# Optimization experiments

Hardware: AMD Instinct MI355X
Metric: run time of the kernel (lower is better)

The kernel has to match this reference:

```python
import jax, jax.numpy as jnp
import numpy as np

HEADS = 8
DIM_HEAD = 64
NB_FEATURES = 256
DIM = 512

def setup_inputs() -> dict:
    key = jax.random.key(0)
    ks = jax.random.split(key, 4)
    b, n = 2, 8192
    x = jax.random.normal(ks[0], (b, n, DIM), jnp.float32)
    # fan-in scaling so exp(feature projections) stays numerically sane
    Wqkv = jax.random.normal(ks[1], (3 * HEADS * DIM_HEAD, DIM), jnp.float32) / np.sqrt(DIM).astype(np.float32)
    Wout = jax.random.normal(ks[2], (DIM, HEADS * DIM_HEAD), jnp.float32) / np.sqrt(HEADS * DIM_HEAD).astype(np.float32)
    bout = jnp.zeros((DIM,), jnp.float32)
    proj = jax.random.normal(ks[3], (NB_FEATURES, DIM_HEAD), jnp.float32) / np.sqrt(DIM_HEAD).astype(np.float32)
    return {"x": x, "Wqkv": Wqkv, "Wout": Wout, "bout": bout, "proj": proj}

def reference(x, Wqkv, Wout, bout, proj):
    b, n, _ = x.shape
    scale = DIM_HEAD ** -0.5
    qkv = jnp.einsum('bnd,ed->bne', x, Wqkv)            # [b,n,3*h*dh]
    q, k, v = jnp.split(qkv, 3, axis=-1)
    to_heads = lambda t: t.reshape(b, n, HEADS, DIM_HEAD).transpose(0, 2, 1, 3)  # [b,h,n,dh]
    q = to_heads(q) * scale
    k = to_heads(k)
    v = to_heads(v)
    # FAVOR+ exp feature maps
    q_prime = jnp.exp(jnp.einsum('bhnd,fd->bhnf', q, proj))  # [b,h,n,f]
    k_prime = jnp.exp(jnp.einsum('bhnd,fd->bhnf', k, proj))  # [b,h,n,f]
    k_sum = k_prime.sum(axis=2)                              # [b,h,f]
    D = jnp.einsum('bhnf,bhf->bhn', q_prime, k_sum)          # normalizer
    D_inv = 1.0 / (D + 1e-6)
    context = jnp.einsum('bhmf,bhmd->bhfd', k_prime, v)      # [b,h,f,dh]
    out = jnp.einsum('bhnf,bhfd->bhnd', q_prime, context) * D_inv[..., None]
    out = out.transpose(0, 2, 1, 3).reshape(b, n, HEADS * DIM_HEAD)
    return jnp.einsum('bne,de->bnd', out, Wout) + bout
```

## Files before the change

### kernel.cpp

```cpp
#include <hip/hip_runtime.h>
#include <math.h>

#define B_    2
#define NSEQ  8192
#define DIM_  512
#define H_    8
#define DH_   64
#define F_    256
#define M_    (B_*NSEQ)
#define QKV_  1536

typedef __attribute__((ext_vector_type(8))) short     short8;
typedef __attribute__((ext_vector_type(4))) float     float4v;
typedef __attribute__((ext_vector_type(8))) unsigned short ushort8v;

__device__ __forceinline__ unsigned short f2bf(float f) {
    unsigned u = __float_as_uint(f);
    u += 0x7FFFu + ((u >> 16) & 1u);
    return (unsigned short)(u >> 16);
}
__device__ __forceinline__ unsigned pack2bf(float lo, float hi) {
    return __builtin_amdgcn_perm(__float_as_uint(hi), __float_as_uint(lo), 0x07060302);
}
__device__ __forceinline__ void glds16(const void* g, void* s) {
    __builtin_amdgcn_global_load_lds(
        (const __attribute__((address_space(1))) unsigned int*)g,
        (__attribute__((address_space(3))) unsigned int*)s, 16, 0, 0);
}

__global__ __launch_bounds__(256) void cvt_all(const float* __restrict__ x,
                                               const float* __restrict__ wqkv,
                                               const float* __restrict__ wout,
                                               const float* __restrict__ proj,
                                               unsigned short* __restrict__ xb,
                                               unsigned short* __restrict__ wqkvb,
                                               unsigned short* __restrict__ woutb,
                                               unsigned short* __restrict__ projb) {
    int bid = blockIdx.x;
    const float* in; unsigned short* out; int i;
    if (bid < 4096)      { in = x;    out = xb;    i = bid * 256 + threadIdx.x; }
    else if (bid < 4480) { in = wqkv; out = wqkvb; i = (bid - 4096) * 256 + threadIdx.x; }
    else if (bid < 4608) { in = wout; out = woutb; i = (bid - 4480) * 256 + threadIdx.x; }
    else                 { in = proj; out = projb; i = (bid - 4608) * 256 + threadIdx.x; }
    float4 a = ((const float4*)in)[2 * i];
    float4 b = ((const float4*)in)[2 * i + 1];
    ushort8v o;
    o[0] = f2bf(a.x); o[1] = f2bf(a.y); o[2] = f2bf(a.z); o[3] = f2bf(a.w);
    o[4] = f2bf(b.x); o[5] = f2bf(b.y); o[6] = f2bf(b.z); o[7] = f2bf(b.w);
    ((ushort8v*)out)[i] = o;
}

template<bool BF16OUT>
__global__ __launch_bounds__(256) void gemm_nt_pp(const unsigned short* __restrict__ A,
                                                  const unsigned short* __restrict__ Bm,
                                                  const float* __restrict__ bias,
                                                  void* __restrict__ Cout,
                                                  int M, int N, int K) {
    __shared__ __align__(16) unsigned short As[2][128 * 32];
    __shared__ __align__(16) unsigned short Bs[2][128 * 32];
    const int t  = threadIdx.x;
    const int w  = t >> 6, l = t & 63;
    const int wm = w >> 1, wn = w & 1;
    const int m0 = blockIdx.y * 128, n0 = blockIdx.x * 128;
    const int lr = l & 15, lq = l >> 4;

    float4v acc[4][4];
#pragma unroll
    for (int mi = 0; mi < 4; mi++)
#pragma unroll
        for (int ni = 0; ni < 4; ni++) acc[mi][ni] = (float4v){0.f, 0.f, 0.f, 0.f};

    auto stage = [&](int buf, int k0) {
#pragma unroll
        for (int i = 0; i < 2; i++) {
            int rb8 = w * 2 + i;
            int row = rb8 * 16 + lr;
            glds16(A + (size_t)(m0 + row) * K + k0 + lq * 8, &As[buf][rb8 * 512]);
            glds16(Bm + (size_t)(n0 + row) * K + k0 + lq * 8, &Bs[buf][rb8 * 512]);
        }
    };

    const int nk = K >> 5;
    stage(0, 0);
    __syncthreads();

    for (int k = 0; k < nk; k++) {
        const int cur = k & 1;
        if (k + 1 < nk) stage(cur ^ 1, (k + 1) << 5);

        short8 af[4], bfr[4];
#pragma unroll
        for (int mi = 0; mi < 4; mi++)
            af[mi] = *(const short8*)&As[cur][((wm * 4 + mi) * 64 + l) * 8];
#pragma unroll
        for (int ni = 0; ni < 4; ni++)
            bfr[ni] = *(const short8*)&Bs[cur][((wn * 4 + ni) * 64 + l) * 8];
#pragma unroll
        for (int mi = 0; mi < 4; mi++)
#pragma unroll
            for (int ni = 0; ni < 4; ni++)
                acc[mi][ni] = __builtin_amdgcn_mfma_f32_16x16x32_bf16(
                    af[mi], bfr[ni], acc[mi][ni], 0, 0, 0);

        if (k + 1 < nk) __syncthreads();
    }

    const int q = l >> 4, c = l & 15;
#pragma unroll
    for (int mi = 0; mi < 4; mi++) {
        int row0 = m0 + wm * 64 + mi * 16 + q * 4;
#pragma unroll
        for (int ni = 0; ni < 4; ni++) {
            int col = n0 + wn * 64 + ni * 16 + c;
            float bv = bias ? bias[col] : 0.f;
#pragma unroll
            for (int r = 0; r < 4; r++) {
                float v = acc[mi][ni][r] + bv;
                if (BF16OUT) ((unsigned short*)Cout)[(size_t)(row0 + r) * N + col] = f2bf(v);
                else         ((float*)Cout)[(size_t)(row0 + r) * N + col] = v;
            }
        }
    }
}

__global__ __launch_bounds__(256) void vtrans(const unsigned short* __restrict__ qkvb,
                                              unsigned short* __restrict__ vT) {
    __shared__ unsigned short T[128][80];
    const int t = threadIdx.x;
    const int n0 = blockIdx.x * 128, z = blockIdx.y;
    const int b = z >> 3, h = z & 7;
#pragma unroll
    for (int i = 0; i < 4; i++) {
        int flat = t + i * 256;
        int n = flat >> 3, d8 = flat & 7;
        ushort8v v = *(const ushort8v*)(qkvb + ((size_t)b * NSEQ + n0 + n) * QKV_ + 1024 + h * 64 + d8 * 8);
        *(ushort8v*)&T[n][d8 * 8] = v;
    }
    __syncthreads();
#pragma unroll
    for (int i = 0; i < 4; i++) {
        int flat = t + i * 256;
        int d = flat >> 4, n8 = flat & 15;
        ushort8v o;
#pragma unroll
        for (int j = 0; j < 8; j++) o[j] = T[n8 * 8 + j][d];
        *(ushort8v*)(vT + ((size_t)z * 64 + d) * NSEQ + n0 + n8 * 8) = o;
    }
}

__global__ __launch_bounds__(256) void ctx_fused_mfma(
    const unsigned short* __restrict__ qkvb,
    const unsigned short* __restrict__ projb,
    const unsigned short* __restrict__ vT,
    float* __restrict__ partial)
{
    __shared__ __align__(16) unsigned short PB[32 * 512];
    __shared__ __align__(16) unsigned short KB[8 * 512];
    __shared__ __align__(16) unsigned short VB[8 * 512];
    __shared__ __align__(16) unsigned short KPA[32 * 512];
    const int t = threadIdx.x, w = t >> 6, l = t & 63;
    const int lr = l & 15, lq = l >> 4;
    const int s = blockIdx.x, z = blockIdx.y;
    const int b = z >> 3, h = z & 7;
    const int nchunk = s * 256;

    for (int idx = w; idx < 32; idx += 4) {
        int fblk = idx >> 1, kt = idx & 1;
        glds16(projb + (size_t)(fblk * 16 + lr) * 64 + kt * 32 + lq * 8, &PB[idx * 512]);
    }

    float4v acc[4][5];
#pragma unroll
    for (int mi = 0; mi < 4; mi++)
#pragma unroll
        for (int ni = 0; ni < 5; ni++) acc[mi][ni] = (float4v){0.f, 0.f, 0.f, 0.f};
    short ov = (lr == 0) ? (short)0x3F80 : (short)0;
    short8 ones = {ov, ov, ov, ov, ov, ov, ov, ov};

    for (int st = 0; st < 4; st++) {
        int nbase = nchunk + st * 64;
        __syncthreads();
        for (int idx = w; idx < 8; idx += 4) {
            int nblk = idx >> 1, kt = idx & 1;
            glds16(qkvb + ((size_t)b * NSEQ + nbase + nblk * 16 + lr) * QKV_ + 512 + h * 64 + kt * 32 + lq * 8,
                   &KB[idx * 512]);
        }
        for (int idx = w; idx < 8; idx += 4) {
            int dhb = idx >> 1, nt2 = idx & 1;
            glds16(vT + ((size_t)z * 64 + dhb * 16 + lr) * NSEQ + nbase + nt2 * 32 + lq * 8,
                   &VB[idx * 512]);
        }
        __syncthreads();

        float4v a2[4][4];
#pragma unroll
        for (int mi = 0; mi < 4; mi++)
#pragma unroll
            for (int ni = 0; ni < 4; ni++) a2[mi][ni] = (float4v){0.f, 0.f, 0.f, 0.f};
#pragma unroll
        for (int ks = 0; ks < 2; ks++) {
            short8 ka[4], pb[4];
#pragma unroll
            for (int mi = 0; mi < 4; mi++)
                ka[mi] = *(const short8*)&KB[((mi * 2 + ks) * 64 + l) * 8];
#pragma unroll
            for (int ni = 0; ni < 4; ni++)
                pb[ni] = *(const short8*)&PB[(((w * 4 + ni) * 2 + ks) * 64 + l) * 8];
#pragma unroll
            for (int mi = 0; mi < 4; mi++)
#pragma unroll
                for (int ni = 0; ni < 4; ni++)
                    a2[mi][ni] = __builtin_amdgcn_mfma_f32_16x16x32_bf16(ka[mi], pb[ni], a2[mi][ni], 0, 0, 0);
        }
#pragma unroll
        for (int mi = 0; mi < 4; mi++) {
            int nb = mi * 16 + lq * 4;
            int qoff = ((nb >> 3) & 3) * 256 + (nb & 7) * 2;
            int setn = nb >> 5;
#pragma unroll
            for (int ni = 0; ni < 4; ni++) {
                int f = w * 64 + ni * 16 + lr;
                float e0 = __expf(a2[mi][ni][0]);
                float e1 = __expf(a2[mi][ni][1]);
                float e2 = __expf(a2[mi][ni][2]);
                float e3 = __expf(a2[mi][ni][3]);
                uint2 p; p.x = pack2bf(e0, e1); p.y = pack2bf(e2, e3);
                *(uint2*)((char*)KPA + (size_t)(((f >> 4) * 2 + setn) * 1024 + qoff + (f & 15) * 16)) = p;
            }
        }
#pragma unroll
        for (int ks = 0; ks < 2; ks++) {
            short8 af[4], bf[4];
#pragma unroll
            for (int mi = 0; mi < 4; mi++)
                af[mi] = *(const short8*)&KPA[(((w * 4 + mi) * 2 + ks) * 64 + l) * 8];
#pragma unroll
            for (int ni = 0; ni < 4; ni++)
                bf[ni] = *(const short8*)&VB[((ni * 2 + ks) * 64 + l) * 8];
#pragma unroll
            for (int mi = 0; mi < 4; mi++) {
#pragma unroll
                for (int ni = 0; ni < 4; ni++)
                    acc[mi][ni] = __builtin_amdgcn_mfma_f32_16x16x32_bf16(af[mi], bf[ni], acc[mi][ni], 0, 0, 0);
                acc[mi][4] = __builtin_amdgcn_mfma_f32_16x16x32_bf16(af[mi], ones, acc[mi][4], 0, 0, 0);
            }
        }
    }
    float* base = partial + (size_t)(s * 16 + z) * 80 * 256;
#pragma unroll
    for (int mi = 0; mi < 4; mi++) {
        int f0r = w * 64 + mi * 16 + lq * 4;
#pragma unroll
        for (int ni = 0; ni < 5; ni++) {
            int col = ni * 16 + lr;
#pragma unroll
            for (int r = 0; r < 4; r++)
                base[(size_t)col * 256 + f0r + r] = acc[mi][ni][r];
        }
    }
}

__global__ __launch_bounds__(256) void ctx_reduce(const float* __restrict__ partial,
                                                  unsigned short* __restrict__ ctxT) {
    int idx = blockIdx.x * 256 + threadIdx.x;
    const int NC = 16 * 80 * 256;
    if (idx >= NC) return;
    float s = 0.f;
#pragma unroll
    for (int k = 0; k < 32; k++) s += partial[(size_t)k * NC + idx];
    ctxT[idx] = f2bf(s);
}

__global__ __launch_bounds__(256) void attn_fused_mfma(
    const unsigned short* __restrict__ qkvb,
    const unsigned short* __restrict__ projb,
    const unsigned short* __restrict__ ctxT,
    unsigned short* __restrict__ attnb)
{
    __shared__ __align__(16) unsigned short QB[16 * 512];
    __shared__ __align__(16) unsigned short PA[8 * 512];
    __shared__ __align__(16) unsigned short QPA[16 * 512];
    __shared__ __align__(16) unsigned short CB[10 * 512];
    const int t = threadIdx.x, w = t >> 6, l = t & 63;
    const int lr = l & 15, lq = l >> 4;
    const int m0 = blockIdx.x * 128, z = blockIdx.y;
    const int b = z >> 3, h = z & 7;

    for (int idx = w; idx < 16; idx += 4) {
        int mblk = idx >> 1, kt = idx & 1;
        glds16(qkvb + ((size_t)b * NSEQ + m0 + mblk * 16 + lr) * QKV_ + h * 64 + kt * 32 + lq * 8,
               &QB[idx * 512]);
    }
    float4v acc[2][5];
#pragma unroll
    for (int mi = 0; mi < 2; mi++)
#pragma unroll
        for (int ni = 0; ni < 5; ni++) acc[mi][ni] = (float4v){0.f, 0.f, 0.f, 0.f};

    for (int fs = 0; fs < 4; fs++) {
        int f0 = fs * 64;
        __syncthreads();
        for (int idx = w; idx < 8; idx += 4) {
            int fb = idx >> 1, kt = idx & 1;
            glds16(projb + (size_t)(f0 + fb * 16 + lr) * 64 + kt * 32 + lq * 8, &PA[idx * 512]);
        }
        for (int idx = w; idx < 10; idx += 4) {
            int dhb = idx >> 1, ft = idx & 1;
            glds16(ctxT + ((size_t)z * 80 + dhb * 16 + lr) * 256 + f0 + ft * 32 + lq * 8,
                   &CB[idx * 512]);
        }
        __syncthreads();

        float4v a2[4][2];
#pragma unroll
        for (int mi = 0; mi < 4; mi++)
#pragma unroll
            for (int ni = 0; ni < 2; ni++) a2[mi][ni] = (float4v){0.f, 0.f, 0.f, 0.f};
#pragma unroll
        for (int ks = 0; ks < 2; ks++) {
            short8 pa[4], qb[2];
#pragma unroll
            for (int mi = 0; mi < 4; mi++)
                pa[mi] = *(const short8*)&PA[((mi * 2 + ks) * 64 + l) * 8];
#pragma unroll
            for (int ni = 0; ni < 2; ni++)
                qb[ni] = *(const short8*)&QB[(((w * 2 + ni) * 2 + ks) * 64 + l) * 8];
#pragma unroll
            for (int mi = 0; mi < 4; mi++)
#pragma unroll
                for (int ni = 0; ni < 2; ni++)
                    a2[mi][ni] = __builtin_amdgcn_mfma_f32_16x16x32_bf16(pa[mi], qb[ni], a2[mi][ni], 0, 0, 0);
        }
#pragma unroll
        for (int mi = 0; mi < 4; mi++) {
            int fb2 = mi * 16 + lq * 4;
            int qoff = ((fb2 >> 3) & 3) * 256 + (fb2 & 7) * 2;
            int setf = fb2 >> 5;
#pragma unroll
            for (int ni = 0; ni < 2; ni++) {
                int m = w * 32 + ni * 16 + lr;
                float e0 = __expf(0.125f * a2[mi][ni][0]);
                float e1 = __expf(0.125f * a2[mi][ni][1]);
                float e2 = __expf(0.125f * a2[mi][ni][2]);
                float e3 = __expf(0.125f * a2[mi][ni][3]);
                uint2 p; p.x = pack2bf(e0, e1); p.y = pack2bf(e2, e3);
                *(uint2*)((char*)QPA + (size_t)(((m >> 4) * 2 + setf) * 1024 + qoff + (m & 15) * 16)) = p;
            }
        }
#pragma unroll
        for (int ks = 0; ks < 2; ks++) {
            short8 af[2], cb[5];
#pragma unroll
            for (int mi = 0; mi < 2; mi++)
                af[mi] = *(const short8*)&QPA[(((w * 2 + mi) * 2 + ks) * 64 + l) * 8];
#pragma unroll
            for (int ni = 0; ni < 5; ni++)
                cb[ni] = *(const short8*)&CB[((ni * 2 + ks) * 64 + l) * 8];
#pragma unroll
            for (int mi = 0; mi < 2; mi++)
#pragma unroll
                for (int ni = 0; ni < 5; ni++)
                    acc[mi][ni] = __builtin_amdgcn_mfma_f32_16x16x32_bf16(af[mi], cb[ni], acc[mi][ni], 0, 0, 0);
        }
    }
#pragma unroll
    for (int mi = 0; mi < 2; mi++) {
        int rowb = m0 + w * 32 + mi * 16 + lq * 4;
#pragma unroll
        for (int r = 0; r < 4; r++) {
            float dv = __shfl(acc[mi][4][r], (l & 48), 64);
            float rinv = 1.f / (dv + 1e-6f);
#pragma unroll
            for (int ni = 0; ni < 4; ni++)
                attnb[((size_t)b * NSEQ + rowb + r) * 512 + h * 64 + ni * 16 + lr] =
                    f2bf(acc[mi][ni][r] * rinv);
        }
    }
}

extern "C" void kernel_launch(void* const* d_in, const int* in_sizes, int n_in,
                              void* d_out, int out_size, void* d_ws, size_t ws_size,
                              hipStream_t stream) {
    const float* x    = (const float*)d_in[0];
    const float* Wqkv = (const float*)d_in[1];
    const float* Wout = (const float*)d_in[2];
    const float* bout = (const float*)d_in[3];
    const float* proj = (const float*)d_in[4];

    unsigned short* qkvb  = (unsigned short*)d_ws;
    unsigned short* vT    = qkvb + (size_t)M_ * QKV_;
    float*          partial = (float*)(vT + (size_t)16 * 64 * NSEQ);
    unsigned short* ctxT  = (unsigned short*)(partial + (size_t)32 * 16 * 80 * 256);
    unsigned short* projb = ctxT + (size_t)16 * 80 * 256;
    unsigned short* xb    = projb + 16384;
    unsigned short* attnb = xb;
    unsigned short* wqkvb = xb + (size_t)M_ * DIM_;
    unsigned short* woutb = wqkvb + (size_t)QKV_ * DIM_;
    float* outp = (float*)d_out;

    cvt_all<<<dim3(4616), 256, 0, stream>>>(x, Wqkv, Wout, proj, xb, wqkvb, woutb, projb);
    gemm_nt_pp<true><<<dim3(QKV_ / 128, M_ / 128), 256, 0, stream>>>(xb, wqkvb, nullptr, qkvb, M_, QKV_, DIM_);
    vtrans<<<dim3(64, 16), 256, 0, stream>>>(qkvb, vT);
    ctx_fused_mfma<<<dim3(32, 16), 256, 0, stream>>>(qkvb, projb, vT, partial);
    ctx_reduce<<<dim3(1280), 256, 0, stream>>>(partial, ctxT);
    attn_fused_mfma<<<dim3(64, 16), 256, 0, stream>>>(qkvb, projb, ctxT, attnb);
    gemm_nt_pp<false><<<dim3(DIM_ / 128, M_ / 128), 256, 0, stream>>>(attnb, woutb, bout, outp, M_, DIM_, DIM_);
}
```

Measured before the change: 229.7 us.

## Split ctx kernel over feature halves, store bf16 partials, swizzle GEMM blocks

The context kernel grid gains a feature-half dimension, so each block handles 128 of the 256 features. This doubles block count and cuts LDS and register use per block, at the cost of recomputing the K loads per half. Partial sums are now stored as bf16 and reduced with 8-wide vector loads, which halves partial-buffer traffic but adds rounding error to the 32-way sum. The GEMM blocks are remapped with an XCD-style swizzle to improve L2 locality across the chiplets.

```diff
diff --git a/kernel.cpp b/kernel.cpp
--- a/kernel.cpp
+++ b/kernel.cpp
@@ -18,6 +18,10 @@
     unsigned u = __float_as_uint(f);
     u += 0x7FFFu + ((u >> 16) & 1u);
     return (unsigned short)(u >> 16);
+}
+__device__ __forceinline__ float bf2f(unsigned short h) {
+    unsigned u = ((unsigned)h) << 16;
+    return __uint_as_float(u);
 }
 __device__ __forceinline__ unsigned pack2bf(float lo, float hi) {
     return __builtin_amdgcn_perm(__float_as_uint(hi), __float_as_uint(lo), 0x07060302);
@@ -61,8 +65,13 @@
     const int t  = threadIdx.x;
     const int w  = t >> 6, l = t & 63;
     const int wm = w >> 1, wn = w & 1;
-    const int m0 = blockIdx.y * 128, n0 = blockIdx.x * 128;
     const int lr = l & 15, lq = l >> 4;
+
+    const int gx = gridDim.x;
+    int flat = blockIdx.y * gx + blockIdx.x;
+    int per  = (gx * gridDim.y) >> 3;
+    int flat2 = (flat & 7) * per + (flat >> 3);
+    const int m0 = (flat2 / gx) * 128, n0 = (flat2 % gx) * 128;
 
     float4v acc[4][4];
 #pragma unroll
@@ -152,26 +161,26 @@
     const unsigned short* __restrict__ qkvb,
     const unsigned short* __restrict__ projb,
     const unsigned short* __restrict__ vT,
-    float* __restrict__ partial)
+    unsigned short* __restrict__ partial)
 {
-    __shared__ __align__(16) unsigned short PB[32 * 512];
+    __shared__ __align__(16) unsigned short PB[16 * 512];
     __shared__ __align__(16) unsigned short KB[8 * 512];
     __shared__ __align__(16) unsigned short VB[8 * 512];
-    __shared__ __align__(16) unsigned short KPA[32 * 512];
+    __shared__ __align__(16) unsigned short KPA[16 * 512];
     const int t = threadIdx.x, w = t >> 6, l = t & 63;
     const int lr = l & 15, lq = l >> 4;
-    const int s = blockIdx.x, z = blockIdx.y;
+    const int s = blockIdx.x, fh = blockIdx.y, z = blockIdx.z;
     const int b = z >> 3, h = z & 7;
     const int nchunk = s * 256;
 
-    for (int idx = w; idx < 32; idx += 4) {
+    for (int idx = w; idx < 16; idx += 4) {
         int fblk = idx >> 1, kt = idx & 1;
-        glds16(projb + (size_t)(fblk * 16 + lr) * 64 + kt * 32 + lq * 8, &PB[idx * 512]);
-    }
-
-    float4v acc[4][5];
-#pragma unroll
-    for (int mi = 0; mi < 4; mi++)
+        glds16(projb + (size_t)(fh * 128 + fblk * 16 + lr) * 64 + kt * 32 + lq * 8, &PB[idx * 512]);
+    }
+
+    float4v acc[2][5];
+#pragma unroll
+    for (int mi = 0; mi < 2; mi++)
 #pragma unroll
         for (int ni = 0; ni < 5; ni++) acc[mi][ni] = (float4v){0.f, 0.f, 0.f, 0.f};
     short ov = (lr == 0) ? (short)0x3F80 : (short)0;
@@ -192,24 +201,24 @@
         }
         __syncthreads();
 
-        float4v a2[4][4];
+        float4v a2[4][2];
 #pragma unroll
         for (int mi = 0; mi < 4; mi++)
 #pragma unroll
-            for (int ni = 0; ni < 4; ni++) a2[mi][ni] = (float4v){0.f, 0.f, 0.f, 0.f};
+            for (int ni = 0; ni < 2; ni++) a2[mi][ni] = (float4v){0.f, 0.f, 0.f, 0.f};
 #pragma unroll
         for (int ks = 0; ks < 2; ks++) {
-            short8 ka[4], pb[4];
+            short8 ka[4], pb[2];
 #pragma unroll
             for (int mi = 0; mi < 4; mi++)
                 ka[mi] = *(const short8*)&KB[((mi * 2 + ks) * 64 + l) * 8];
 #pragma unroll
-            for (int ni = 0; ni < 4; ni++)
-                pb[ni] = *(const short8*)&PB[(((w * 4 + ni) * 2 + ks) * 64 + l) * 8];
+            for (int ni = 0; ni < 2; ni++)
+                pb[ni] = *(const short8*)&PB[(((w * 2 + ni) * 2 + ks) * 64 + l) * 8];
 #pragma unroll
             for (int mi = 0; mi < 4; mi++)
 #pragma unroll
-                for (int ni = 0; ni < 4; ni++)
+                for (int ni = 0; ni < 2; ni++)
                     a2[mi][ni] = __builtin_amdgcn_mfma_f32_16x16x32_bf16(ka[mi], pb[ni], a2[mi][ni], 0, 0, 0);
         }
 #pragma unroll
@@ -218,27 +227,27 @@
             int qoff = ((nb >> 3) & 3) * 256 + (nb & 7) * 2;
             int setn = nb >> 5;
 #pragma unroll
-            for (int ni = 0; ni < 4; ni++) {
-                int f = w * 64 + ni * 16 + lr;
+            for (int ni = 0; ni < 2; ni++) {
+                int fp = w * 32 + ni * 16 + lr;
                 float e0 = __expf(a2[mi][ni][0]);
                 float e1 = __expf(a2[mi][ni][1]);
                 float e2 = __expf(a2[mi][ni][2]);
                 float e3 = __expf(a2[mi][ni][3]);
                 uint2 p; p.x = pack2bf(e0, e1); p.y = pack2bf(e2, e3);
-                *(uint2*)((char*)KPA + (size_t)(((f >> 4) * 2 + setn) * 1024 + qoff + (f & 15) * 16)) = p;
+                *(uint2*)((char*)KPA + (size_t)(((fp >> 4) * 2 + setn) * 1024 + qoff + (fp & 15) * 16)) = p;
             }
         }
 #pragma unroll
         for (int ks = 0; ks < 2; ks++) {
-            short8 af[4], bf[4];
-#pragma unroll
-            for (int mi = 0; mi < 4; mi++)
-                af[mi] = *(const short8*)&KPA[(((w * 4 + mi) * 2 + ks) * 64 + l) * 8];
+            short8 af[2], bf[4];
+#pragma unroll
+            for (int mi = 0; mi < 2; mi++)
+                af[mi] = *(const short8*)&KPA[(((w * 2 + mi) * 2 + ks) * 64 + l) * 8];
 #pragma unroll
             for (int ni = 0; ni < 4; ni++)
                 bf[ni] = *(const short8*)&VB[((ni * 2 + ks) * 64 + l) * 8];
 #pragma unroll
-            for (int mi = 0; mi < 4; mi++) {
+            for (int mi = 0; mi < 2; mi++) {
 #pragma unroll
                 for (int ni = 0; ni < 4; ni++)
                     acc[mi][ni] = __builtin_amdgcn_mfma_f32_16x16x32_bf16(af[mi], bf[ni], acc[mi][ni], 0, 0, 0);
@@ -246,29 +255,36 @@
             }
         }
     }
-    float* base = partial + (size_t)(s * 16 + z) * 80 * 256;
-#pragma unroll
-    for (int mi = 0; mi < 4; mi++) {
-        int f0r = w * 64 + mi * 16 + lq * 4;
+    unsigned short* base = partial + (size_t)(s * 16 + z) * 80 * 256 + fh * 128;
+#pragma unroll
+    for (int mi = 0; mi < 2; mi++) {
+        int f0r = w * 32 + mi * 16 + lq * 4;
 #pragma unroll
         for (int ni = 0; ni < 5; ni++) {
             int col = ni * 16 + lr;
 #pragma unroll
             for (int r = 0; r < 4; r++)
-                base[(size_t)col * 256 + f0r + r] = acc[mi][ni][r];
-        }
-    }
-}
-
-__global__ __launch_bounds__(256) void ctx_reduce(const float* __restrict__ partial,
+                base[(size_t)col * 256 + f0r + r] = f2bf(acc[mi][ni][r]);
+        }
+    }
+}
+
+__global__ __launch_bounds__(256) void ctx_reduce(const unsigned short* __restrict__ partial,
                                                   unsigned short* __restrict__ ctxT) {
-    int idx = blockIdx.x * 256 + threadIdx.x;
-    const int NC = 16 * 80 * 256;
-    if (idx >= NC) return;
-    float s = 0.f;
-#pragma unroll
-    for (int k = 0; k < 32; k++) s += partial[(size_t)k * NC + idx];
-    ctxT[idx] = f2bf(s);
+    int idx8 = blockIdx.x * 256 + threadIdx.x;
+    const int INNER = 16 * 80 * 256;
+    size_t off = (size_t)idx8 * 8;
+    float s0 = 0.f, s1 = 0.f, s2 = 0.f, s3 = 0.f, s4 = 0.f, s5 = 0.f, s6 = 0.f, s7 = 0.f;
+#pragma unroll
+    for (int k = 0; k < 32; k++) {
+        ushort8v v = *(const ushort8v*)(partial + (size_t)k * INNER + off);
+        s0 += bf2f(v[0]); s1 += bf2f(v[1]); s2 += bf2f(v[2]); s3 += bf2f(v[3]);
+        s4 += bf2f(v[4]); s5 += bf2f(v[5]); s6 += bf2f(v[6]); s7 += bf2f(v[7]);
+    }
+    ushort8v o;
+    o[0] = f2bf(s0); o[1] = f2bf(s1); o[2] = f2bf(s2); o[3] = f2bf(s3);
+    o[4] = f2bf(s4); o[5] = f2bf(s5); o[6] = f2bf(s6); o[7] = f2bf(s7);
+    *(ushort8v*)(ctxT + off) = o;
 }
 
 __global__ __launch_bounds__(256) void attn_fused_mfma(
@@ -387,22 +403,22 @@
     const float* bout = (const float*)d_in[3];
     const float* proj = (const float*)d_in[4];
 
-    unsigned short* qkvb  = (unsigned short*)d_ws;
-    unsigned short* vT    = qkvb + (size_t)M_ * QKV_;
-    float*          partial = (float*)(vT + (size_t)16 * 64 * NSEQ);
-    unsigned short* ctxT  = (unsigned short*)(partial + (size_t)32 * 16 * 80 * 256);
-    unsigned short* projb = ctxT + (size_t)16 * 80 * 256;
-    unsigned short* xb    = projb + 16384;
-    unsigned short* attnb = xb;
-    unsigned short* wqkvb = xb + (size_t)M_ * DIM_;
-    unsigned short* woutb = wqkvb + (size_t)QKV_ * DIM_;
+    unsigned short* qkvb    = (unsigned short*)d_ws;
+    unsigned short* vT      = qkvb + (size_t)M_ * QKV_;
+    unsigned short* partial = vT + (size_t)16 * 64 * NSEQ;
+    unsigned short* ctxT    = partial + (size_t)32 * 16 * 80 * 256;
+    unsigned short* projb   = ctxT + (size_t)16 * 80 * 256;
+    unsigned short* xb      = projb + 16384;
+    unsigned short* attnb   = xb;
+    unsigned short* wqkvb   = xb + (size_t)M_ * DIM_;
+    unsigned short* woutb   = wqkvb + (size_t)QKV_ * DIM_;
     float* outp = (float*)d_out;
 
     cvt_all<<<dim3(4616), 256, 0, stream>>>(x, Wqkv, Wout, proj, xb, wqkvb, woutb, projb);
     gemm_nt_pp<true><<<dim3(QKV_ / 128, M_ / 128), 256, 0, stream>>>(xb, wqkvb, nullptr, qkvb, M_, QKV_, DIM_);
     vtrans<<<dim3(64, 16), 256, 0, stream>>>(qkvb, vT);
-    ctx_fused_mfma<<<dim3(32, 16), 256, 0, stream>>>(qkvb, projb, vT, partial);
-    ctx_reduce<<<dim3(1280), 256, 0, stream>>>(partial, ctxT);
+    ctx_fused_mfma<<<dim3(32, 2, 16), 256, 0, stream>>>(qkvb, projb, vT, partial);
+    ctx_reduce<<<dim3(160), 256, 0, stream>>>(partial, ctxT);
     attn_fused_mfma<<<dim3(64, 16), 256, 0, stream>>>(qkvb, projb, ctxT, attnb);
     gemm_nt_pp<false><<<dim3(DIM_ / 128, M_ / 128), 256, 0, stream>>>(attnb, woutb, bout, outp, M_, DIM_, DIM_);
 }
```

Result: faster. 224.6 us (-2.2%).
